# Optimization experiments

Measured on AMD Instinct MI355X. Metric: run time of the kernel, lower is better.

## Reference

```python
import jax, jax.numpy as jnp
import numpy as np

EMBED_DIM = 768
NUM_HEADS = 12
HEAD_DIM = EMBED_DIM // NUM_HEADS
SCALE = HEAD_DIM ** -0.5
EPS = 1e-5


def _layernorm(x, g, b):
    m = jnp.mean(x, axis=-1, keepdims=True)
    v = jnp.mean(jnp.square(x - m), axis=-1, keepdims=True)
    return (x - m) * jax.lax.rsqrt(v + EPS) * g + b


def setup_inputs() -> dict:
    key = jax.random.key(0)
    ks = jax.random.split(key, 8)
    B, N, D, Hd = 16, 1024, EMBED_DIM, HEAD_DIM
    x = jax.random.normal(ks[0], (B, N, D), dtype=jnp.float32)
    W_qkv = jax.random.normal(ks[1], (D, 3 * D), dtype=jnp.float32) * (D ** -0.5)
    b_qkv = jnp.zeros((3 * D,), dtype=jnp.float32)
    W_proj = jax.random.normal(ks[2], (D, D), dtype=jnp.float32) * (D ** -0.5)
    b_proj = jnp.zeros((D,), dtype=jnp.float32)
    return {
        "x": x,
        "ln_g": jnp.ones((D,), jnp.float32), "ln_b": jnp.zeros((D,), jnp.float32),
        "W_qkv": W_qkv, "b_qkv": b_qkv,
        "qn_g": jnp.ones((Hd,), jnp.float32), "qn_b": jnp.zeros((Hd,), jnp.float32),
        "kn_g": jnp.ones((Hd,), jnp.float32), "kn_b": jnp.zeros((Hd,), jnp.float32),
        "W_proj": W_proj, "b_proj": b_proj,
    }


def reference(x, ln_g, ln_b, W_qkv, b_qkv, qn_g, qn_b, kn_g, kn_b, W_proj, b_proj):
    B, N, D = x.shape
    H, Hd = NUM_HEADS, HEAD_DIM
    xn = _layernorm(x, ln_g, ln_b)                      # qkv_norm (pre-LN of embed_dim)
    qkv = xn @ W_qkv + b_qkv                            # [B,N,3D]
    qkv = qkv.reshape(B, N, 3, H, Hd)
    q = jnp.transpose(qkv[:, :, 0], (0, 2, 1, 3))       # [B,H,N,Hd]
    k = jnp.transpose(qkv[:, :, 1], (0, 2, 1, 3))
    v = jnp.transpose(qkv[:, :, 2], (0, 2, 1, 3))
    q = _layernorm(q, qn_g, qn_b)                       # per-head QK LayerNorm
    k = _layernorm(k, kn_g, kn_b)
    attn = jnp.einsum("bhnd,bhmd->bhnm", q, k) * SCALE
    attn = jax.nn.softmax(attn, axis=-1)
    out = jnp.einsum("bhnm,bhmd->bhnd", attn, v)        # [B,H,N,Hd]
    out = jnp.transpose(out, (0, 2, 1, 3)).reshape(B, N, D)
    return out @ W_proj + b_proj
```

## Files before the change

kernel.cpp:

```cpp
#include <hip/hip_runtime.h>

typedef _Float16 half8 __attribute__((ext_vector_type(8)));
typedef _Float16 half4 __attribute__((ext_vector_type(4)));
typedef float f32x4 __attribute__((ext_vector_type(4)));

#define B_    16
#define N_    1024
#define D_    768
#define H_    12
#define M_    (B_ * N_)
#define QKVN_ 2304
#define EPS_  1e-5f
#define QS_   0.18033688011112042f

__device__ __forceinline__ float exp2_fast(float x) {
#if __has_builtin(__builtin_amdgcn_exp2f)
    return __builtin_amdgcn_exp2f(x);
#else
    return __builtin_exp2f(x);
#endif
}

__device__ __forceinline__ void gl16(const _Float16* g, _Float16* l) {
    __builtin_amdgcn_global_load_lds((const __attribute__((address_space(1))) void*)g,
                                     (__attribute__((address_space(3))) void*)l, 16, 0, 0);
}

__global__ __launch_bounds__(256) void convert_w(const float* __restrict__ Wqkv,
                                                 const float* __restrict__ Wproj,
                                                 _Float16* __restrict__ wqkvT,
                                                 _Float16* __restrict__ wprojT) {
    __shared__ float T[64][65];
    int t = blockIdx.x;
    const float* W; _Float16* O; int NW, k0, n0;
    if (t < 432) { W = Wqkv;  O = wqkvT;  NW = QKVN_; k0 = (t % 12) * 64; n0 = (t / 12) * 64; }
    else { t -= 432; W = Wproj; O = wprojT; NW = D_;  k0 = (t % 12) * 64; n0 = (t / 12) * 64; }
    int c = threadIdx.x & 63, r4 = threadIdx.x >> 6;
#pragma unroll
    for (int i = 0; i < 16; ++i) {
        int r = i * 4 + r4;
        T[r][c] = W[(size_t)(k0 + r) * NW + n0 + c];
    }
    __syncthreads();
#pragma unroll
    for (int i = 0; i < 16; ++i) {
        int r = i * 4 + r4;
        O[(size_t)(n0 + r) * D_ + k0 + c] = (_Float16)T[c][r];
    }
}

__global__ __launch_bounds__(256) void ln_embed(const float* __restrict__ x,
                                                const float* __restrict__ g,
                                                const float* __restrict__ bb,
                                                _Float16* __restrict__ xn) {
    int row = blockIdx.x;
    int tid = threadIdx.x;
    const float* xr = x + (size_t)row * D_;
    float v0 = xr[tid], v1 = xr[tid + 256], v2 = xr[tid + 512];
    float s = v0 + v1 + v2;
    float q = v0 * v0 + v1 * v1 + v2 * v2;
#pragma unroll
    for (int m = 32; m >= 1; m >>= 1) {
        s += __shfl_xor(s, m);
        q += __shfl_xor(q, m);
    }
    __shared__ float ss[4], qq[4];
    int wave = tid >> 6;
    if ((tid & 63) == 0) { ss[wave] = s; qq[wave] = q; }
    __syncthreads();
    float S = ss[0] + ss[1] + ss[2] + ss[3];
    float Q = qq[0] + qq[1] + qq[2] + qq[3];
    float mean = S * (1.f / 768.f);
    float var  = Q * (1.f / 768.f) - mean * mean;
    float rstd = rsqrtf(var + EPS_);
    _Float16* xo = xn + (size_t)row * D_;
    xo[tid]       = (_Float16)((v0 - mean) * rstd * g[tid]       + bb[tid]);
    xo[tid + 256] = (_Float16)((v1 - mean) * rstd * g[tid + 256] + bb[tid + 256]);
    xo[tid + 512] = (_Float16)((v2 - mean) * rstd * g[tid + 512] + bb[tid + 512]);
}

__global__ __launch_bounds__(256) void gemm_qkv(const _Float16* __restrict__ A,
                                                const _Float16* __restrict__ BT,
                                                const float* __restrict__ bias,
                                                const float* __restrict__ qn_g,
                                                const float* __restrict__ qn_b,
                                                const float* __restrict__ kn_g,
                                                const float* __restrict__ kn_b,
                                                _Float16* __restrict__ qo,
                                                _Float16* __restrict__ ko,
                                                _Float16* __restrict__ vt) {
    __shared__ _Float16 As[2][128 * 32];
    __shared__ _Float16 Bs[2][128 * 32];
    const int K = D_;
    int xcd = blockIdx.x & 7, loc = blockIdx.x >> 3;
    int m0 = (xcd * 16 + loc / 18) * 128;
    int n0 = (loc % 18) * 128;
    int tid = threadIdx.x;
    int wave = tid >> 6, lane = tid & 63;
    int wm = wave >> 1, wn = wave & 1;
    int lg = lane >> 4, l15 = lane & 15;
    int xorr = (l15 >> 1) & 3;

    auto stage = [&](int b, int k0) {
#pragma unroll
        for (int i = 0; i < 2; ++i) {
            int cb = (i * 4 + wave) * 64;
            int chunk = cb + lane;
            int r = chunk >> 2, c = chunk & 3;
            int cg = c ^ ((r >> 1) & 3);
            gl16(&A[(size_t)(m0 + r) * K + k0 + cg * 8], &As[b][cb * 8]);
            gl16(&BT[(size_t)(n0 + r) * K + k0 + cg * 8], &Bs[b][cb * 8]);
        }
    };

    f32x4 acc[4][4] = {};
    stage(0, 0);
    __syncthreads();
    for (int t = 0; t < 24; ++t) {
        int cur = t & 1;
        if (t < 23) stage(cur ^ 1, (t + 1) * 32);
        half8 af[4], bf[4];
#pragma unroll
        for (int i = 0; i < 4; ++i) {
            af[i] = *(const half8*)&As[cur][(wm * 64 + i * 16 + l15) * 32 + (lg ^ xorr) * 8];
            bf[i] = *(const half8*)&Bs[cur][(wn * 64 + i * 16 + l15) * 32 + (lg ^ xorr) * 8];
        }
#pragma unroll
        for (int mi = 0; mi < 4; ++mi)
#pragma unroll
            for (int ni = 0; ni < 4; ++ni)
                acc[mi][ni] = __builtin_amdgcn_mfma_f32_16x16x32_f16(af[mi], bf[ni], acc[mi][ni], 0, 0, 0);
        __syncthreads();
    }

    int col0 = n0 + wn * 64;
    int s = col0 / 768;
    int hcol = (col0 % 768) >> 6;
    float qkvb[4];
#pragma unroll
    for (int ni = 0; ni < 4; ++ni) qkvb[ni] = bias[col0 + ni * 16 + l15];

    if (s == 2) {
#pragma unroll
        for (int mi = 0; mi < 4; ++mi) {
            int r0 = m0 + wm * 64 + mi * 16 + lg * 4;
            int bidx = r0 >> 10, pos = r0 & 1023;
            int kvblk = pos >> 5, h = (pos >> 4) & 1, lgR = (pos >> 2) & 3;
            size_t vbase = ((size_t)(bidx * H_ + hcol) * 32 + kvblk) * 4;
#pragma unroll
            for (int ni = 0; ni < 4; ++ni) {
                half4 h4;
#pragma unroll
                for (int j = 0; j < 4; ++j) h4[j] = (_Float16)(acc[mi][ni][j] + qkvb[ni]);
                *(half4*)&vt[(vbase + ni) * 512 + lgR * 128 + l15 * 8 + h * 4] = h4;
            }
        }
    } else {
        const float* gg = (s == 0) ? qn_g : kn_g;
        const float* bb = (s == 0) ? qn_b : kn_b;
        float gv[4], bv[4];
#pragma unroll
        for (int ni = 0; ni < 4; ++ni) { gv[ni] = gg[ni * 16 + l15]; bv[ni] = bb[ni * 16 + l15]; }
#pragma unroll
        for (int mi = 0; mi < 4; ++mi) {
#pragma unroll
            for (int j = 0; j < 4; ++j) {
                float v[4];
                float sm = 0.f, sq = 0.f;
#pragma unroll
                for (int ni = 0; ni < 4; ++ni) {
                    v[ni] = acc[mi][ni][j] + qkvb[ni];
                    sm += v[ni];
                    sq += v[ni] * v[ni];
                }
#pragma unroll
                for (int msk = 1; msk < 16; msk <<= 1) {
                    sm += __shfl_xor(sm, msk);
                    sq += __shfl_xor(sq, msk);
                }
                float mean = sm * (1.f / 64.f);
                float var  = sq * (1.f / 64.f) - mean * mean;
                float rstd = rsqrtf(var + EPS_);
                int row = m0 + wm * 64 + mi * 16 + lg * 4 + j;
                int bidx = row >> 10, pos = row & 1023;
                if (s == 0) {
                    size_t rbase = ((size_t)(bidx * H_ + hcol) * 1024 + pos) * 64;
#pragma unroll
                    for (int ni = 0; ni < 4; ++ni) {
                        float o = (v[ni] - mean) * rstd * gv[ni] + bv[ni];
                        qo[rbase + ni * 16 + l15] = (_Float16)(o * QS_);
                    }
                } else {
                    int kvblk = pos >> 5, nh = (pos >> 4) & 1, l15R = pos & 15;
                    size_t base2 = ((size_t)(bidx * H_ + hcol) * 32 + kvblk) * 4 + nh * 2;
#pragma unroll
                    for (int ni = 0; ni < 4; ++ni) {
                        float o = (v[ni] - mean) * rstd * gv[ni] + bv[ni];
                        int ks = ni >> 1, lgR = ((ni & 1) << 1) | (l15 >> 3), elem = l15 & 7;
                        ko[(base2 + ks) * 512 + lgR * 128 + l15R * 8 + elem] = (_Float16)o;
                    }
                }
            }
        }
    }
}

struct KV {
    half8 kf[2][2];
    half8 vf[4];
};

__device__ __forceinline__ void ldKV(KV& s, const _Float16* kp, const _Float16* vp, int kvblk) {
    const _Float16* kb = kp + (size_t)kvblk * 2048;
#pragma unroll
    for (int nh = 0; nh < 2; ++nh)
#pragma unroll
        for (int ks = 0; ks < 2; ++ks)
            s.kf[nh][ks] = *(const half8*)(kb + (nh * 2 + ks) * 512);
    const _Float16* vb = vp + (size_t)kvblk * 2048;
#pragma unroll
    for (int di = 0; di < 4; ++di)
        s.vf[di] = *(const half8*)(vb + di * 512);
}

__device__ __forceinline__ void blockKV(const KV& s, const half8 (&qf)[4][2],
                                        f32x4 (&oacc)[4][4], f32x4 (&lacc)[4],
                                        half8 ones) {
#pragma unroll
    for (int mi = 0; mi < 4; ++mi) {
        f32x4 a0 = {}, a1 = {};
#pragma unroll
        for (int ks = 0; ks < 2; ++ks) {
            a0 = __builtin_amdgcn_mfma_f32_16x16x32_f16(s.kf[0][ks], qf[mi][ks], a0, 0, 0, 0);
            a1 = __builtin_amdgcn_mfma_f32_16x16x32_f16(s.kf[1][ks], qf[mi][ks], a1, 0, 0, 0);
        }
        half8 pf;
#pragma unroll
        for (int j = 0; j < 4; ++j) {
            pf[j]     = (_Float16)exp2_fast(a0[j]);
            pf[j + 4] = (_Float16)exp2_fast(a1[j]);
        }
        lacc[mi] = __builtin_amdgcn_mfma_f32_16x16x32_f16(ones, pf, lacc[mi], 0, 0, 0);
#pragma unroll
        for (int di = 0; di < 4; ++di)
            oacc[mi][di] = __builtin_amdgcn_mfma_f32_16x16x32_f16(s.vf[di], pf, oacc[mi][di], 0, 0, 0);
    }
}

__global__ __launch_bounds__(128, 2) void attn(const _Float16* __restrict__ qg,
                                               const _Float16* __restrict__ kg,
                                               const _Float16* __restrict__ vtg,
                                               _Float16* __restrict__ o) {
    int bphys = blockIdx.x;
    int jj = (bphys & 7) * 192 + (bphys >> 3);
    int bh = jj >> 3, qt = jj & 7;
    int b = bh / H_, h = bh % H_;
    int tid = threadIdx.x;
    int wid = tid >> 6, lane = tid & 63;
    int lg = lane >> 4, l15 = lane & 15;
    size_t base = (size_t)bh << 10;
    int qw0 = qt * 128 + wid * 64;

    const _Float16* qrow = qg + (base + qw0 + l15) * 64 + lg * 8;
    half8 qf[4][2];
#pragma unroll
    for (int mi = 0; mi < 4; ++mi)
#pragma unroll
        for (int ks = 0; ks < 2; ++ks)
            qf[mi][ks] = *(const half8*)(qrow + mi * 1024 + ks * 32);

    const _Float16* kp = kg + (size_t)bh * 65536 + lane * 8;
    const _Float16* vp = vtg + (size_t)bh * 65536 + lane * 8;

    half8 ones;
#pragma unroll
    for (int i = 0; i < 8; ++i) ones[i] = (_Float16)1.0f;

    f32x4 oacc[4][4] = {};
    f32x4 lacc[4] = {};

    KV s0, s1;
    ldKV(s0, kp, vp, 0);
    for (int t = 0; t < 16; ++t) {
        ldKV(s1, kp, vp, (2 * t + 1) & 31);
        blockKV(s0, qf, oacc, lacc, ones);
        ldKV(s0, kp, vp, (2 * t + 2) & 31);
        blockKV(s1, qf, oacc, lacc, ones);
    }

#pragma unroll
    for (int mi = 0; mi < 4; ++mi) {
        float inv = 1.f / lacc[mi][0];
        int q = qw0 + mi * 16 + l15;
        size_t rowb = ((size_t)(b * N_ + q)) * D_ + h * 64 + lg * 4;
#pragma unroll
        for (int di = 0; di < 4; ++di) {
            half4 h4;
#pragma unroll
            for (int j = 0; j < 4; ++j) h4[j] = (_Float16)(oacc[mi][di][j] * inv);
            *(half4*)&o[rowb + di * 16] = h4;
        }
    }
}

__global__ __launch_bounds__(256) void gemm_proj(const _Float16* __restrict__ A,
                                                 const _Float16* __restrict__ BT,
                                                 const float* __restrict__ bias,
                                                 float* __restrict__ out) {
    __shared__ _Float16 As[2][128 * 32];
    __shared__ _Float16 Bs[2][128 * 32];
    const int K = D_;
    int xcd = blockIdx.x & 7, loc = blockIdx.x >> 3;
    int m0 = (xcd * 16 + loc / 6) * 128;
    int n0 = (loc % 6) * 128;
    int tid = threadIdx.x;
    int wave = tid >> 6, lane = tid & 63;
    int wm = wave >> 1, wn = wave & 1;
    int lg = lane >> 4, l15 = lane & 15;
    int xorr = (l15 >> 1) & 3;

    auto stage = [&](int b, int k0) {
#pragma unroll
        for (int i = 0; i < 2; ++i) {
            int cb = (i * 4 + wave) * 64;
            int chunk = cb + lane;
            int r = chunk >> 2, c = chunk & 3;
            int cg = c ^ ((r >> 1) & 3);
            gl16(&A[(size_t)(m0 + r) * K + k0 + cg * 8], &As[b][cb * 8]);
            gl16(&BT[(size_t)(n0 + r) * K + k0 + cg * 8], &Bs[b][cb * 8]);
        }
    };

    f32x4 acc[4][4] = {};
    stage(0, 0);
    __syncthreads();
    for (int t = 0; t < 24; ++t) {
        int cur = t & 1;
        if (t < 23) stage(cur ^ 1, (t + 1) * 32);
        half8 af[4], bf[4];
#pragma unroll
        for (int i = 0; i < 4; ++i) {
            af[i] = *(const half8*)&As[cur][(wm * 64 + i * 16 + l15) * 32 + (lg ^ xorr) * 8];
            bf[i] = *(const half8*)&Bs[cur][(wn * 64 + i * 16 + l15) * 32 + (lg ^ xorr) * 8];
        }
#pragma unroll
        for (int mi = 0; mi < 4; ++mi)
#pragma unroll
            for (int ni = 0; ni < 4; ++ni)
                acc[mi][ni] = __builtin_amdgcn_mfma_f32_16x16x32_f16(af[mi], bf[ni], acc[mi][ni], 0, 0, 0);
        __syncthreads();
    }
#pragma unroll
    for (int mi = 0; mi < 4; ++mi)
#pragma unroll
        for (int ni = 0; ni < 4; ++ni) {
            int col = n0 + wn * 64 + ni * 16 + l15;
            float bv = bias[col];
#pragma unroll
            for (int j = 0; j < 4; ++j) {
                int row = m0 + wm * 64 + mi * 16 + lg * 4 + j;
                out[(size_t)row * D_ + col] = acc[mi][ni][j] + bv;
            }
        }
}

extern "C" void kernel_launch(void* const* d_in, const int* in_sizes, int n_in,
                              void* d_out, int out_size, void* d_ws, size_t ws_size,
                              hipStream_t stream) {
    const float* x      = (const float*)d_in[0];
    const float* ln_g   = (const float*)d_in[1];
    const float* ln_b   = (const float*)d_in[2];
    const float* W_qkv  = (const float*)d_in[3];
    const float* b_qkv  = (const float*)d_in[4];
    const float* qn_g   = (const float*)d_in[5];
    const float* qn_b   = (const float*)d_in[6];
    const float* kn_g   = (const float*)d_in[7];
    const float* kn_b   = (const float*)d_in[8];
    const float* W_proj = (const float*)d_in[9];
    const float* b_proj = (const float*)d_in[10];
    float* out = (float*)d_out;
    char* ws = (char*)d_ws;

    constexpr size_t XN_SZ    = (size_t)M_ * D_ * 2;
    constexpr size_t WQKVT_SZ = (size_t)QKVN_ * D_ * 2;
    constexpr size_t WPROJT_SZ= (size_t)D_ * D_ * 2;
    constexpr size_t HEAD_SZ  = (size_t)B_ * H_ * N_ * 64 * 2;

    _Float16* xn     = (_Float16*)(ws);
    _Float16* wqkvT  = (_Float16*)(ws + XN_SZ);
    _Float16* wprojT = (_Float16*)(ws + XN_SZ + WQKVT_SZ);
    _Float16* qb     = (_Float16*)(ws + XN_SZ + WQKVT_SZ + WPROJT_SZ);
    _Float16* kb     = (_Float16*)((char*)qb + HEAD_SZ);
    _Float16* vtb    = (_Float16*)((char*)kb + HEAD_SZ);
    _Float16* ao     = xn;

    convert_w<<<576, 256, 0, stream>>>(W_qkv, W_proj, wqkvT, wprojT);
    ln_embed<<<M_, 256, 0, stream>>>(x, ln_g, ln_b, xn);
    gemm_qkv<<<M_ / 128 * (QKVN_ / 128), 256, 0, stream>>>(xn, wqkvT, b_qkv,
                                                           qn_g, qn_b, kn_g, kn_b,
                                                           qb, kb, vtb);
    attn<<<B_ * H_ * (N_ / 128), 128, 0, stream>>>(qb, kb, vtb, ao);
    gemm_proj<<<M_ / 128 * (D_ / 128), 256, 0, stream>>>(ao, wprojT, b_proj, out);
}
```

Measured before the change: 226.3 us.

## Triple-buffer LDS staging in QKV and projection GEMMs; vectorize embed LayerNorm

Both GEMM kernels move from double to triple LDS buffering. Three k-tiles are prefetched up front, and a manual vmcnt wait plus raw barriers replace __syncthreads, so global loads stay two tiles ahead of the MFMA work. The aim is to hide global memory latency better, at the cost of more LDS per block, which may lower occupancy. The loop also issues redundant wrap-around loads, (t+3)%24, in its last iterations. The embed LayerNorm is rewritten to use float2 loads and half2 stores.

```diff
diff --git a/kernel.cpp b/kernel.cpp
--- a/kernel.cpp
+++ b/kernel.cpp
@@ -2,6 +2,7 @@
 
 typedef _Float16 half8 __attribute__((ext_vector_type(8)));
 typedef _Float16 half4 __attribute__((ext_vector_type(4)));
+typedef _Float16 half2v __attribute__((ext_vector_type(2)));
 typedef float f32x4 __attribute__((ext_vector_type(4)));
 
 #define B_    16
@@ -55,10 +56,12 @@
                                                 _Float16* __restrict__ xn) {
     int row = blockIdx.x;
     int tid = threadIdx.x;
-    const float* xr = x + (size_t)row * D_;
-    float v0 = xr[tid], v1 = xr[tid + 256], v2 = xr[tid + 512];
-    float s = v0 + v1 + v2;
-    float q = v0 * v0 + v1 * v1 + v2 * v2;
+    const float2* xr = (const float2*)(x + (size_t)row * D_);
+    float2 v0 = xr[tid];
+    float2 v1 = make_float2(0.f, 0.f);
+    if (tid < 128) v1 = xr[256 + tid];
+    float s = v0.x + v0.y + v1.x + v1.y;
+    float q = v0.x * v0.x + v0.y * v0.y + v1.x * v1.x + v1.y * v1.y;
 #pragma unroll
     for (int m = 32; m >= 1; m >>= 1) {
         s += __shfl_xor(s, m);
@@ -73,10 +76,23 @@
     float mean = S * (1.f / 768.f);
     float var  = Q * (1.f / 768.f) - mean * mean;
     float rstd = rsqrtf(var + EPS_);
-    _Float16* xo = xn + (size_t)row * D_;
-    xo[tid]       = (_Float16)((v0 - mean) * rstd * g[tid]       + bb[tid]);
-    xo[tid + 256] = (_Float16)((v1 - mean) * rstd * g[tid + 256] + bb[tid + 256]);
-    xo[tid + 512] = (_Float16)((v2 - mean) * rstd * g[tid + 512] + bb[tid + 512]);
+    const float2* g2 = (const float2*)g;
+    const float2* b2 = (const float2*)bb;
+    half2v* xo = (half2v*)(xn + (size_t)row * D_);
+    {
+        float2 ga = g2[tid], ba = b2[tid];
+        half2v w;
+        w[0] = (_Float16)((v0.x - mean) * rstd * ga.x + ba.x);
+        w[1] = (_Float16)((v0.y - mean) * rstd * ga.y + ba.y);
+        xo[tid] = w;
+    }
+    if (tid < 128) {
+        float2 ga = g2[256 + tid], ba = b2[256 + tid];
+        half2v w;
+        w[0] = (_Float16)((v1.x - mean) * rstd * ga.x + ba.x);
+        w[1] = (_Float16)((v1.y - mean) * rstd * ga.y + ba.y);
+        xo[256 + tid] = w;
+    }
 }
 
 __global__ __launch_bounds__(256) void gemm_qkv(const _Float16* __restrict__ A,
@@ -89,8 +105,8 @@
                                                 _Float16* __restrict__ qo,
                                                 _Float16* __restrict__ ko,
                                                 _Float16* __restrict__ vt) {
-    __shared__ _Float16 As[2][128 * 32];
-    __shared__ _Float16 Bs[2][128 * 32];
+    __shared__ _Float16 As[3][128 * 32];
+    __shared__ _Float16 Bs[3][128 * 32];
     const int K = D_;
     int xcd = blockIdx.x & 7, loc = blockIdx.x >> 3;
     int m0 = (xcd * 16 + loc / 18) * 128;
@@ -101,36 +117,41 @@
     int lg = lane >> 4, l15 = lane & 15;
     int xorr = (l15 >> 1) & 3;
 
-    auto stage = [&](int b, int k0) {
+    auto stage = [&](int buf, int tstep) {
+        int k0 = tstep * 32;
 #pragma unroll
         for (int i = 0; i < 2; ++i) {
             int cb = (i * 4 + wave) * 64;
             int chunk = cb + lane;
             int r = chunk >> 2, c = chunk & 3;
             int cg = c ^ ((r >> 1) & 3);
-            gl16(&A[(size_t)(m0 + r) * K + k0 + cg * 8], &As[b][cb * 8]);
-            gl16(&BT[(size_t)(n0 + r) * K + k0 + cg * 8], &Bs[b][cb * 8]);
+            gl16(&A[(size_t)(m0 + r) * K + k0 + cg * 8], &As[buf][cb * 8]);
+            gl16(&BT[(size_t)(n0 + r) * K + k0 + cg * 8], &Bs[buf][cb * 8]);
         }
     };
 
     f32x4 acc[4][4] = {};
-    stage(0, 0);
-    __syncthreads();
+    stage(0, 0); stage(1, 1); stage(2, 2);
     for (int t = 0; t < 24; ++t) {
-        int cur = t & 1;
-        if (t < 23) stage(cur ^ 1, (t + 1) * 32);
+        int cur = t % 3;
+        asm volatile("s_waitcnt vmcnt(8)" ::: "memory");
+        __builtin_amdgcn_s_barrier();
+        const _Float16* asb = As[cur];
+        const _Float16* bsb = Bs[cur];
         half8 af[4], bf[4];
 #pragma unroll
         for (int i = 0; i < 4; ++i) {
-            af[i] = *(const half8*)&As[cur][(wm * 64 + i * 16 + l15) * 32 + (lg ^ xorr) * 8];
-            bf[i] = *(const half8*)&Bs[cur][(wn * 64 + i * 16 + l15) * 32 + (lg ^ xorr) * 8];
+            af[i] = *(const half8*)&asb[(wm * 64 + i * 16 + l15) * 32 + (lg ^ xorr) * 8];
+            bf[i] = *(const half8*)&bsb[(wn * 64 + i * 16 + l15) * 32 + (lg ^ xorr) * 8];
         }
 #pragma unroll
         for (int mi = 0; mi < 4; ++mi)
 #pragma unroll
             for (int ni = 0; ni < 4; ++ni)
                 acc[mi][ni] = __builtin_amdgcn_mfma_f32_16x16x32_f16(af[mi], bf[ni], acc[mi][ni], 0, 0, 0);
-        __syncthreads();
+        __builtin_amdgcn_sched_barrier(0);
+        __builtin_amdgcn_s_barrier();
+        stage(cur, (t + 3) % 24);
     }
 
     int col0 = n0 + wn * 64;
@@ -307,8 +328,8 @@
                                                  const _Float16* __restrict__ BT,
                                                  const float* __restrict__ bias,
                                                  float* __restrict__ out) {
-    __shared__ _Float16 As[2][128 * 32];
-    __shared__ _Float16 Bs[2][128 * 32];
+    __shared__ _Float16 As[3][128 * 32];
+    __shared__ _Float16 Bs[3][128 * 32];
     const int K = D_;
     int xcd = blockIdx.x & 7, loc = blockIdx.x >> 3;
     int m0 = (xcd * 16 + loc / 6) * 128;
@@ -319,36 +340,41 @@
     int lg = lane >> 4, l15 = lane & 15;
     int xorr = (l15 >> 1) & 3;
 
-    auto stage = [&](int b, int k0) {
+    auto stage = [&](int buf, int tstep) {
+        int k0 = tstep * 32;
 #pragma unroll
         for (int i = 0; i < 2; ++i) {
             int cb = (i * 4 + wave) * 64;
             int chunk = cb + lane;
             int r = chunk >> 2, c = chunk & 3;
             int cg = c ^ ((r >> 1) & 3);
-            gl16(&A[(size_t)(m0 + r) * K + k0 + cg * 8], &As[b][cb * 8]);
-            gl16(&BT[(size_t)(n0 + r) * K + k0 + cg * 8], &Bs[b][cb * 8]);
+            gl16(&A[(size_t)(m0 + r) * K + k0 + cg * 8], &As[buf][cb * 8]);
+            gl16(&BT[(size_t)(n0 + r) * K + k0 + cg * 8], &Bs[buf][cb * 8]);
         }
     };
 
     f32x4 acc[4][4] = {};
-    stage(0, 0);
-    __syncthreads();
+    stage(0, 0); stage(1, 1); stage(2, 2);
     for (int t = 0; t < 24; ++t) {
-        int cur = t & 1;
-        if (t < 23) stage(cur ^ 1, (t + 1) * 32);
+        int cur = t % 3;
+        asm volatile("s_waitcnt vmcnt(8)" ::: "memory");
+        __builtin_amdgcn_s_barrier();
+        const _Float16* asb = As[cur];
+        const _Float16* bsb = Bs[cur];
         half8 af[4], bf[4];
 #pragma unroll
         for (int i = 0; i < 4; ++i) {
-            af[i] = *(const half8*)&As[cur][(wm * 64 + i * 16 + l15) * 32 + (lg ^ xorr) * 8];
-            bf[i] = *(const half8*)&Bs[cur][(wn * 64 + i * 16 + l15) * 32 + (lg ^ xorr) * 8];
+            af[i] = *(const half8*)&asb[(wm * 64 + i * 16 + l15) * 32 + (lg ^ xorr) * 8];
+            bf[i] = *(const half8*)&bsb[(wn * 64 + i * 16 + l15) * 32 + (lg ^ xorr) * 8];
         }
 #pragma unroll
         for (int mi = 0; mi < 4; ++mi)
 #pragma unroll
             for (int ni = 0; ni < 4; ++ni)
                 acc[mi][ni] = __builtin_amdgcn_mfma_f32_16x16x32_f16(af[mi], bf[ni], acc[mi][ni], 0, 0, 0);
-        __syncthreads();
+        __builtin_amdgcn_sched_barrier(0);
+        __builtin_amdgcn_s_barrier();
+        stage(cur, (t + 3) % 24);
     }
 #pragma unroll
     for (int mi = 0; mi < 4; ++mi)
```

Measured after the change: 234.2 us. 3.5% more time.
